# Optimization experiments

Hardware: AMD Instinct MI355X
Metric: run time of the kernel (lower is better)

Reference implementation:

```python
import jax, jax.numpy as jnp
import numpy as np
import math

N_RAYS = 262144
HASHMAP_SIZE = 2 ** 19          # log2_hashmap_size = 19 (default)
BASE_RES = 16
FINEST_RES = 512
N_LEVELS = 4
N_FEATS = 2
_b = math.exp((math.log(FINEST_RES) - math.log(BASE_RES)) / (N_LEVELS - 1))
RESOLUTIONS = [int(math.floor(BASE_RES * _b ** l)) for l in range(N_LEVELS)]  # [16, 50, 161, 512]
PRIMES = jnp.array([1, 2654435761], dtype=jnp.uint32)
CORNERS = jnp.array([[0, 0], [0, 1], [1, 0], [1, 1]], dtype=jnp.uint32)  # 2^dim corners
DIM = 256
N_MID = 6  # n_layers=8 -> 1 input + 6 hidden + 1 output linear


def _hash_level(x, table, resolution):
    # x: [N,2] in [0,1]; table: [HASHMAP_SIZE, N_FEATS]
    xf = x * resolution
    xi = jnp.floor(xf)
    f = xf - xi                                   # [N,2] fractional part
    idx = xi.astype(jnp.uint32)[:, None, :] + CORNERS[None]  # [N,4,2]
    h = idx * PRIMES                              # uint32 wraps mod 2^32
    h = (h[..., 0] ^ h[..., 1]) % HASHMAP_SIZE    # [N,4] spatial hash
    vals = table[h]                               # [N,4,F] gather
    fx, fy = f[:, 0:1], f[:, 1:2]
    w = jnp.concatenate([(1 - fx) * (1 - fy), (1 - fx) * fy,
                         fx * (1 - fy), fx * fy], axis=-1)  # [N,4] bilinear weights
    return jnp.einsum('nc,ncf->nf', w, vals)      # [N,F]


def _encode(x, tables):
    # tables: [N_LEVELS, HASHMAP_SIZE, N_FEATS]
    return jnp.concatenate([_hash_level(x, tables[l], RESOLUTIONS[l])
                            for l in range(N_LEVELS)], axis=-1)  # [N, 8]


def setup_inputs() -> dict:
    key = jax.random.key(0)
    ks = jax.random.split(key, 8)
    s_in = 1.0 / math.sqrt(16)
    s_mid = 1.0 / math.sqrt(DIM)
    return {
        'x': jax.random.uniform(ks[0], (N_RAYS, 4), dtype=jnp.float32),
        'table1': jax.random.normal(ks[1], (N_LEVELS, HASHMAP_SIZE, N_FEATS), dtype=jnp.float32) * 1e-4,
        'table2': jax.random.normal(ks[2], (N_LEVELS, HASHMAP_SIZE, N_FEATS), dtype=jnp.float32) * 1e-4,
        'W_in': jax.random.normal(ks[3], (16, DIM), dtype=jnp.float32) * s_in,
        'b_in': jnp.zeros((DIM,), dtype=jnp.float32),
        'W_mid': jax.random.normal(ks[4], (N_MID, DIM, DIM), dtype=jnp.float32) * s_mid,
        'b_mid': jnp.zeros((N_MID, DIM), dtype=jnp.float32),
        'W_out': jax.random.normal(ks[5], (DIM, 1), dtype=jnp.float32) * s_mid,
        'b_out': jnp.zeros((1,), dtype=jnp.float32),
    }


def reference(x, table1, table2, W_in, b_in, W_mid, b_mid, W_out, b_out):
    # ray2param runs under torch.no_grad(): block gradients to x
    x = jax.lax.stop_gradient(x)
    emb = jnp.concatenate([_encode(x[:, :2], table1),
                           _encode(x[:, 2:], table2)], axis=-1)  # [N,16]
    h = emb @ W_in + b_in                         # LazyLinear(16 -> 256)
    for i in range(N_MID):                        # fixed 6 hidden layers
        h = jax.nn.relu(h) @ W_mid[i] + b_mid[i]
    return jax.nn.relu(h) @ W_out + b_out         # [N,1]
```

## Files before the change

kernel.cpp:

```cpp
#include <hip/hip_runtime.h>
#include <type_traits>
#include <cmath>
#include <cstdint>

#define NRAYS     262144
#define HASHMAP   524288
#define DIM       256
#define NMID      6
#define MBLK      64
#define ALPHA     512.0f
#define INV_ALPHA (1.0f / 512.0f)

typedef _Float16 half8 __attribute__((ext_vector_type(8)));
typedef _Float16 half2 __attribute__((ext_vector_type(2)));
typedef float  floatx4 __attribute__((ext_vector_type(4)));

#define WIN_ELEMS   8192
#define WL_ELEMS    65536
#define WKC_ELEMS   8192
#define WNC_ELEMS   512

__device__ __forceinline__ int sw_idx(int r, int k) {
  int s = (r ^ (r >> 1)) & 7;
  return (r << 8) + ((((k >> 3) ^ s) << 3) | (k & 7));
}

__global__ __launch_bounds__(256) void prep_weights(
    const float* __restrict__ W_in, const float* __restrict__ W_mid,
    _Float16* __restrict__ wsh)
{
  int tid = blockIdx.x * 256 + threadIdx.x;
  int pos = tid & 511;
  int lane = pos >> 3, j = pos & 7;
  int kk = ((lane >> 4) << 3) + j;
  if (tid < WIN_ELEMS) {
    int nc = tid >> 9;
    int n = (nc << 4) + (lane & 15);
    float v = (kk < 16) ? W_in[kk * DIM + n] : 0.f;
    wsh[nc * WNC_ELEMS + pos] = (_Float16)v;
  } else if (tid < WIN_ELEMS + 6 * WL_ELEMS) {
    int u = tid - WIN_ELEMS;
    int fid = u >> 9;
    int L   = fid >> 7;
    int rem = fid & 127;
    int kc  = rem >> 4;
    int nc  = rem & 15;
    int k = (kc << 5) + kk;
    int n = (nc << 4) + (lane & 15);
    float v = W_mid[L * (DIM * DIM) + k * DIM + n];
    wsh[WIN_ELEMS + L * WL_ELEMS + kc * WKC_ELEMS + nc * WNC_ELEMS + pos] = (_Float16)v;
  }
}

__global__ __launch_bounds__(256, 4) void mlp_fused(
    const float* __restrict__ x,
    const float* __restrict__ table1,
    const float* __restrict__ table2,
    const _Float16* __restrict__ wsh,
    const float* __restrict__ b_in,
    const float* __restrict__ b_mid,
    const float* __restrict__ W_out,
    const float* __restrict__ b_out,
    float* __restrict__ out,
    int res0, int res1, int res2, int res3)
{
  __shared__ __align__(16) _Float16 hs[MBLK * 256];

  const int tid  = threadIdx.x;
  const int lane = tid & 63;
  const int wave = tid >> 6;
  const int col  = lane & 15;
  const int quad = lane >> 4;
  const int rbase = blockIdx.x * MBLK;

  #pragma unroll
  for (int i = 0; i < 2; ++i) {
    int task = tid + (i << 8);
    int r   = task & 63;
    int el  = task >> 6;
    int enc = el >> 2, lev = el & 3;
    const float* xp = x + (size_t)(rbase + r) * 4 + enc * 2;
    float px = xp[0], py = xp[1];
    int res = (lev == 0) ? res0 : (lev == 1) ? res1 : (lev == 2) ? res2 : res3;
    float fres = (float)res;
    float xf = px * fres, yf = py * fres;
    float xi = floorf(xf), yi = floorf(yf);
    float fx = xf - xi,  fy = yf - yi;
    uint32_t ix = (uint32_t)xi, iy = (uint32_t)yi;
    const float2* tab = (const float2*)(enc ? table2 : table1) + (size_t)lev * HASHMAP;
    float f0 = 0.f, f1 = 0.f;
    #pragma unroll
    for (int c = 0; c < 4; ++c) {
      uint32_t c0 = (uint32_t)(c >> 1), c1 = (uint32_t)(c & 1);
      uint32_t h = ((ix + c0) ^ ((iy + c1) * 2654435761u)) & (uint32_t)(HASHMAP - 1);
      float2 v = tab[h];
      float w = (c0 ? fx : 1.f - fx) * (c1 ? fy : 1.f - fy);
      f0 += w * v.x;
      f1 += w * v.y;
    }
    int cb = enc * 8 + lev * 2;
    half2 hp = {(_Float16)(f0 * ALPHA), (_Float16)(f1 * ALPHA)};
    *(half2*)&hs[sw_idx(r, cb)] = hp;
  }
  for (int i = tid; i < MBLK * 16; i += 256) {
    int r = i >> 4, k = 16 + (i & 15);
    hs[sw_idx(r, k)] = (_Float16)0.f;
  }
  __syncthreads();

  floatx4 acc[4][4];

  const int s_a = (col ^ (col >> 1)) & 7;
  const int s2  = (s_a >> 2) & 1;
  const int abase = col * 512 + (quad ^ (s_a & 3)) * 16;
  const char* const hsb = (const char*)hs;

  auto run_layer = [&](auto kc_const, const _Float16* __restrict__ wbase,
                       const float* __restrict__ bias_ptr) {
    constexpr int KCOUNT = decltype(kc_const)::value;

    {
      float bv[4];
      #pragma unroll
      for (int nl = 0; nl < 4; ++nl)
        bv[nl] = bias_ptr[wave * 64 + nl * 16 + col] * ALPHA;
      #pragma unroll
      for (int mt = 0; mt < 4; ++mt)
        #pragma unroll
        for (int nl = 0; nl < 4; ++nl)
          acc[mt][nl] = (floatx4){bv[nl], bv[nl], bv[nl], bv[nl]};
    }

    const _Float16* wlane = wbase + wave * 4 * WNC_ELEMS + lane * 8;

    #pragma clang loop unroll(disable)
    for (int kc = 0; kc < KCOUNT; ++kc) {
      half8 b[4];
      const _Float16* wk = wlane + kc * WKC_ELEMS;
      #pragma unroll
      for (int nl = 0; nl < 4; ++nl)
        b[nl] = *(const half8*)(wk + nl * WNC_ELEMS);
      half8 a[4];
      const char* ap = hsb + abase + ((kc ^ s2) << 6);
      #pragma unroll
      for (int mt = 0; mt < 4; ++mt)
        a[mt] = *(const half8*)(ap + mt * 8192);
      __builtin_amdgcn_s_setprio(1);
      #pragma unroll
      for (int nl = 0; nl < 4; ++nl)
        #pragma unroll
        for (int mt = 0; mt < 4; ++mt)
          acc[mt][nl] = __builtin_amdgcn_mfma_f32_16x16x32_f16(a[mt], b[nl], acc[mt][nl], 0, 0, 0);
      __builtin_amdgcn_s_setprio(0);
    }
    __syncthreads();

    {
      const int c3   = (col >> 3) & 1;
      const int ebase = wave * 128 + ((col & 7) << 1);
      #pragma unroll
      for (int nl = 0; nl < 4; ++nl) {
        #pragma unroll
        for (int r = 0; r < 4; ++r) {
          int m0  = quad * 4 + r;
          int s_r = (m0 ^ (m0 >> 1)) & 7;
          int va  = m0 * 512 + ebase + (((((nl << 1) | c3)) ^ s_r) << 4);
          char* wp = (char*)hs + va;
          #pragma unroll
          for (int mt = 0; mt < 4; ++mt) {
            float hv = fmaxf(acc[mt][nl][r], 0.f);
            *(_Float16*)(wp + mt * 8192) = (_Float16)hv;
          }
        }
      }
    }
    __syncthreads();
  };

  run_layer(std::integral_constant<int, 1>{}, wsh, b_in);
  #pragma clang loop unroll(disable)
  for (int L = 0; L < NMID; ++L)
    run_layer(std::integral_constant<int, 8>{}, wsh + WIN_ELEMS + L * WL_ELEMS, b_mid + L * DIM);

  {
    int m = tid >> 2, seg = tid & 3;
    float sum = 0.f;
    #pragma unroll
    for (int i = 0; i < 8; ++i) {
      int k = (seg << 6) + (i << 3);
      half8 hv = *(const half8*)&hs[sw_idx(m, k)];
      float4 w0 = *(const float4*)&W_out[k];
      float4 w1 = *(const float4*)&W_out[k + 4];
      sum += (float)hv[0] * w0.x + (float)hv[1] * w0.y
           + (float)hv[2] * w0.z + (float)hv[3] * w0.w
           + (float)hv[4] * w1.x + (float)hv[5] * w1.y
           + (float)hv[6] * w1.z + (float)hv[7] * w1.w;
    }
    sum += __shfl_xor(sum, 1);
    sum += __shfl_xor(sum, 2);
    if (seg == 0) out[rbase + m] = sum * INV_ALPHA + b_out[0];
  }
}

extern "C" void kernel_launch(void* const* d_in, const int* in_sizes, int n_in,
                              void* d_out, int out_size, void* d_ws, size_t ws_size,
                              hipStream_t stream)
{
  const float* x      = (const float*)d_in[0];
  const float* table1 = (const float*)d_in[1];
  const float* table2 = (const float*)d_in[2];
  const float* W_in   = (const float*)d_in[3];
  const float* b_in   = (const float*)d_in[4];
  const float* W_mid  = (const float*)d_in[5];
  const float* b_mid  = (const float*)d_in[6];
  const float* W_out  = (const float*)d_in[7];
  const float* b_out  = (const float*)d_in[8];
  float* out  = (float*)d_out;
  _Float16* wsh = (_Float16*)d_ws;

  double b = exp((log(512.0) - log(16.0)) / 3.0);
  int res[4];
  for (int l = 0; l < 4; ++l) res[l] = (int)floor(16.0 * pow(b, (double)l));

  int prep_total = WIN_ELEMS + 6 * WL_ELEMS;
  prep_weights<<<prep_total / 256, 256, 0, stream>>>(W_in, W_mid, wsh);
  mlp_fused<<<NRAYS / MBLK, 256, 0, stream>>>(x, table1, table2, wsh, b_in, b_mid,
                                              W_out, b_out, out,
                                              res[0], res[1], res[2], res[3]);
}
```

Measured before the change: 293.2 us.

## Stage weight chunks into LDS via async global_load_lds with one-ahead prefetch

Instead of each wave loading its MFMA B operands straight from global memory every k-chunk, weights are copied asynchronously into a per-wave LDS staging buffer with global_load_lds. The next chunk, or the first chunk of the next layer, is prefetched while the current MFMAs run. The intent is to hide global load latency behind compute. The cost is 16KB of extra LDS per block, which may lower occupancy, and explicit vmcnt/lgkmcnt waits that serialize each iteration.

```diff
diff --git a/kernel.cpp b/kernel.cpp
--- a/kernel.cpp
+++ b/kernel.cpp
@@ -14,6 +14,8 @@
 typedef _Float16 half8 __attribute__((ext_vector_type(8)));
 typedef _Float16 half2 __attribute__((ext_vector_type(2)));
 typedef float  floatx4 __attribute__((ext_vector_type(4)));
+typedef __attribute__((address_space(3))) uint32_t lds_u32_t;
+typedef __attribute__((address_space(1))) uint32_t gbl_u32_t;
 
 #define WIN_ELEMS   8192
 #define WL_ELEMS    65536
@@ -65,6 +67,7 @@
     int res0, int res1, int res2, int res3)
 {
   __shared__ __align__(16) _Float16 hs[MBLK * 256];
+  __shared__ __align__(16) _Float16 wstage[4 * 2048];
 
   const int tid  = threadIdx.x;
   const int lane = tid & 63;
@@ -72,6 +75,16 @@
   const int col  = lane & 15;
   const int quad = lane >> 4;
   const int rbase = blockIdx.x * MBLK;
+
+  auto stage4 = [&](const _Float16* __restrict__ wk) {
+    const _Float16* src = wk + wave * 2048 + lane * 8;
+    _Float16* dst = &wstage[wave * 2048];
+    #pragma unroll
+    for (int nl = 0; nl < 4; ++nl)
+      __builtin_amdgcn_global_load_lds((gbl_u32_t*)(src + nl * WNC_ELEMS),
+                                       (lds_u32_t*)(dst + nl * WNC_ELEMS),
+                                       16, 0, 0);
+  };
 
   #pragma unroll
   for (int i = 0; i < 2; ++i) {
@@ -106,6 +119,7 @@
     int r = i >> 4, k = 16 + (i & 15);
     hs[sw_idx(r, k)] = (_Float16)0.f;
   }
+  stage4(wsh);
   __syncthreads();
 
   floatx4 acc[4][4];
@@ -114,9 +128,11 @@
   const int s2  = (s_a >> 2) & 1;
   const int abase = col * 512 + (quad ^ (s_a & 3)) * 16;
   const char* const hsb = (const char*)hs;
+  const _Float16* const bsrc = &wstage[wave * 2048 + lane * 8];
 
   auto run_layer = [&](auto kc_const, const _Float16* __restrict__ wbase,
-                       const float* __restrict__ bias_ptr) {
+                       const float* __restrict__ bias_ptr,
+                       const _Float16* __restrict__ next_wbase) {
     constexpr int KCOUNT = decltype(kc_const)::value;
 
     {
@@ -131,20 +147,21 @@
           acc[mt][nl] = (floatx4){bv[nl], bv[nl], bv[nl], bv[nl]};
     }
 
-    const _Float16* wlane = wbase + wave * 4 * WNC_ELEMS + lane * 8;
-
     #pragma clang loop unroll(disable)
     for (int kc = 0; kc < KCOUNT; ++kc) {
+      asm volatile("s_waitcnt vmcnt(0)" ::: "memory");
       half8 b[4];
-      const _Float16* wk = wlane + kc * WKC_ELEMS;
       #pragma unroll
       for (int nl = 0; nl < 4; ++nl)
-        b[nl] = *(const half8*)(wk + nl * WNC_ELEMS);
+        b[nl] = *(const half8*)(bsrc + nl * WNC_ELEMS);
       half8 a[4];
       const char* ap = hsb + abase + ((kc ^ s2) << 6);
       #pragma unroll
       for (int mt = 0; mt < 4; ++mt)
         a[mt] = *(const half8*)(ap + mt * 8192);
+      asm volatile("s_waitcnt lgkmcnt(0)" ::: "memory");
+      if (kc + 1 < KCOUNT)
+        stage4(wbase + (kc + 1) * WKC_ELEMS);
       __builtin_amdgcn_s_setprio(1);
       #pragma unroll
       for (int nl = 0; nl < 4; ++nl)
@@ -153,6 +170,7 @@
           acc[mt][nl] = __builtin_amdgcn_mfma_f32_16x16x32_f16(a[mt], b[nl], acc[mt][nl], 0, 0, 0);
       __builtin_amdgcn_s_setprio(0);
     }
+    if (next_wbase) stage4(next_wbase);
     __syncthreads();
 
     {
@@ -177,10 +195,12 @@
     __syncthreads();
   };
 
-  run_layer(std::integral_constant<int, 1>{}, wsh, b_in);
+  run_layer(std::integral_constant<int, 1>{}, wsh, b_in, wsh + WIN_ELEMS);
   #pragma clang loop unroll(disable)
   for (int L = 0; L < NMID; ++L)
-    run_layer(std::integral_constant<int, 8>{}, wsh + WIN_ELEMS + L * WL_ELEMS, b_mid + L * DIM);
+    run_layer(std::integral_constant<int, 8>{}, wsh + WIN_ELEMS + L * WL_ELEMS,
+              b_mid + L * DIM,
+              (L < NMID - 1) ? (wsh + WIN_ELEMS + (L + 1) * WL_ELEMS) : nullptr);
 
   {
     int m = tid >> 2, seg = tid & 3;
```

Result: slower. 362.6 us (+23.7%).
